# Optimization experiments

Measured on AMD Instinct MI355X. Metric: run time of the kernel, lower is better.

The kernel has to match this reference:

```python
import jax, jax.numpy as jnp
import numpy as np

N, E, IN_C, HID, OUT_C, L = 50000, 800000, 256, 96, 64, 3
DELTAS = (1.0, 0.5, 0.25)


def setup_inputs() -> dict:
    key = jax.random.key(0)
    ks = jax.random.split(key, 10)
    x = jax.random.normal(ks[0], (N, IN_C), dtype=jnp.float32)
    edge_index = jax.random.randint(ks[1], (2, E), 0, N, dtype=jnp.int64)
    s = 1.0 / np.sqrt(IN_C)
    proj_w = jax.random.uniform(ks[2], (IN_C, HID), jnp.float32, -s, s)
    proj_b = jax.random.uniform(ks[3], (HID,), jnp.float32, -s, s)
    sh = 1.0 / np.sqrt(HID)
    conv_w = jax.random.uniform(ks[4], (L, HID, HID), jnp.float32, -sh, sh)
    conv_b = jnp.zeros((L, HID), dtype=jnp.float32)
    so = 1.0 / np.sqrt(2 * HID)
    out_w = jax.random.uniform(ks[5], (2 * HID, OUT_C), jnp.float32, -so, so)
    out_b = jax.random.uniform(ks[6], (OUT_C,), jnp.float32, -so, so)
    # dithered-quantization uniform noise in (-0.5, 0.5), per layer
    b_noise = jax.random.uniform(ks[7], (L, N, HID), jnp.float32) - 0.5
    # additive gaussian noise, per layer
    eps_noise = jax.random.normal(ks[8], (L, N, HID), dtype=jnp.float32) * 0.01
    return {
        "x": x, "edge_index": edge_index,
        "proj_w": proj_w, "proj_b": proj_b,
        "conv_w": conv_w, "conv_b": conv_b,
        "out_w": out_w, "out_b": out_b,
        "b_noise": b_noise, "eps_noise": eps_noise,
    }


def _gcn_norm(edge_index, n):
    # add self-loops and compute symmetric normalization (PyG gcn_norm)
    loops = jnp.arange(n, dtype=edge_index.dtype)
    src = jnp.concatenate([edge_index[0], loops])
    dst = jnp.concatenate([edge_index[1], loops])
    deg = jax.ops.segment_sum(jnp.ones_like(dst, dtype=jnp.float32), dst, num_segments=n)
    dis = jnp.where(deg > 0, jax.lax.rsqrt(jnp.maximum(deg, 1.0)), 0.0)
    norm = dis[src] * dis[dst]  # [E+N]
    return src, dst, norm


def reference(x, edge_index, proj_w, proj_b, conv_w, conv_b, out_w, out_b, b_noise, eps_noise):
    n = x.shape[0]
    src, dst, norm = _gcn_norm(edge_index, n)
    h0 = x @ proj_w + proj_b  # [N, HID]
    h = h0
    for k in range(L):
        delta = DELTAS[k]
        b = b_noise[k] * delta
        h_q = jnp.floor((h + b) / delta) * delta - b  # dithered quantize
        m = h_q @ conv_w[k]                           # [N, HID]
        agg = jax.ops.segment_sum(m[src] * norm[:, None], dst, num_segments=n)
        h = jax.nn.relu(agg + conv_b[k] + eps_noise[k])
    return jnp.concatenate([h0, h], axis=-1) @ out_w + out_b
```

## Files before the change

### kernel.cpp

```cpp
#include <hip/hip_runtime.h>
#include <math.h>

#define N_NODES 50000
#define N_EDGES 800000
#define IN_C    256
#define HID     96
#define OUT_C   64
#define NLAYER  3
#define KC      96
#define XSP     100


__global__ void k_init(int* cnt, int* cur, int* counter,
                       int* col, float* wgt, int n) {
    int v = blockIdx.x * blockDim.x + threadIdx.x;
    if (v < n) { cnt[v] = 0; cur[v] = 0; }
    if (v == 0) *counter = 0;
    if (v < 8) { col[N_EDGES + v] = 0; wgt[N_EDGES + v] = 0.f; }
}

__global__ void k_count(const int* __restrict__ ei, int* cnt, int e) {
    int i = blockIdx.x * blockDim.x + threadIdx.x;
    if (i < e) atomicAdd(&cnt[ei[e + i]], 1);
}

__global__ void k_node(const int* __restrict__ cnt, float* __restrict__ dis,
                       int* __restrict__ start, int* counter, int n) {
    int v = blockIdx.x * blockDim.x + threadIdx.x;
    if (v < n) {
        int c = cnt[v];
        dis[v] = (float)(1.0 / sqrt((double)(c + 1)));
        start[v] = atomicAdd(counter, c);
    }
}

__global__ void k_fill(const int* __restrict__ ei, const float* __restrict__ dis,
                       const int* __restrict__ start, int* __restrict__ cur,
                       int* __restrict__ col, float* __restrict__ wgt, int e) {
    int i = blockIdx.x * blockDim.x + threadIdx.x;
    if (i < e) {
        int s = ei[i];
        int d = ei[e + i];
        int slot = start[d] + atomicAdd(&cur[d], 1);
        col[slot] = s;
        wgt[slot] = dis[s] * dis[d];
    }
}


template<bool QUANT, bool BIAS>
__global__ __launch_bounds__(384) void k_gemm(
    const float* __restrict__ A, int lda, int K,
    const float* __restrict__ bn, float delta, float inv_delta,
    const float* __restrict__ W, const float* __restrict__ bias,
    float* __restrict__ C)
{
    __shared__ float xs[64 * XSP];
    const int t  = threadIdx.x;
    const int og = t % 24;
    const int rg = t / 24;
    const int nch = (K + KC - 1) / KC;
    const int ngroups = (N_NODES + 63) / 64;

    const float* Wt = W + 4 * og;

    float4 bv = make_float4(0.f, 0.f, 0.f, 0.f);
    if (BIAS) bv = *(const float4*)&bias[4 * og];

    for (int g = blockIdx.x; g < ngroups; g += gridDim.x) {
        float acc[4][4];
        #pragma unroll
        for (int r = 0; r < 4; r++)
            #pragma unroll
            for (int o = 0; o < 4; o++) acc[r][o] = 0.f;

        for (int ch = 0; ch < nch; ch++) {
            const int kc0 = ch * KC;
            const int kcw = (K - kc0 < KC) ? (K - kc0) : KC;
            __syncthreads();
            const int kq4 = kcw >> 2;
            const int tot = 64 * kq4;
            for (int i = t; i < tot; i += 384) {
                int node, kq;
                if (kq4 == 24) { node = i / 24; kq = i - node * 24; }
                else           { node = i >> 4; kq = i & 15; }
                int gn = g * 64 + node;
                float4 v = make_float4(0.f, 0.f, 0.f, 0.f);
                if (gn < N_NODES) {
                    v = *(const float4*)&A[(size_t)gn * lda + kc0 + 4 * kq];
                    if (QUANT) {
                        float4 b = *(const float4*)&bn[(size_t)gn * HID + kc0 + 4 * kq];
                        float bx = b.x * delta, by = b.y * delta;
                        float bz = b.z * delta, bw = b.w * delta;
                        v.x = floorf((v.x + bx) * inv_delta) * delta - bx;
                        v.y = floorf((v.y + by) * inv_delta) * delta - by;
                        v.z = floorf((v.z + bz) * inv_delta) * delta - bz;
                        v.w = floorf((v.w + bw) * inv_delta) * delta - bw;
                    }
                }
                *(float4*)&xs[node * XSP + 4 * kq] = v;
            }
            __syncthreads();
            const float* Wc = Wt + (size_t)kc0 * HID;
            for (int k = 0; k < kcw; k += 4) {
                float4 w0 = *(const float4*)&Wc[(size_t)(k + 0) * HID];
                float4 w1 = *(const float4*)&Wc[(size_t)(k + 1) * HID];
                float4 w2 = *(const float4*)&Wc[(size_t)(k + 2) * HID];
                float4 w3 = *(const float4*)&Wc[(size_t)(k + 3) * HID];
                #pragma unroll
                for (int r = 0; r < 4; r++) {
                    float4 xv = *(const float4*)&xs[(4 * rg + r) * XSP + k];
                    acc[r][0] = fmaf(xv.x, w0.x, acc[r][0]);
                    acc[r][1] = fmaf(xv.x, w0.y, acc[r][1]);
                    acc[r][2] = fmaf(xv.x, w0.z, acc[r][2]);
                    acc[r][3] = fmaf(xv.x, w0.w, acc[r][3]);
                    acc[r][0] = fmaf(xv.y, w1.x, acc[r][0]);
                    acc[r][1] = fmaf(xv.y, w1.y, acc[r][1]);
                    acc[r][2] = fmaf(xv.y, w1.z, acc[r][2]);
                    acc[r][3] = fmaf(xv.y, w1.w, acc[r][3]);
                    acc[r][0] = fmaf(xv.z, w2.x, acc[r][0]);
                    acc[r][1] = fmaf(xv.z, w2.y, acc[r][1]);
                    acc[r][2] = fmaf(xv.z, w2.z, acc[r][2]);
                    acc[r][3] = fmaf(xv.z, w2.w, acc[r][3]);
                    acc[r][0] = fmaf(xv.w, w3.x, acc[r][0]);
                    acc[r][1] = fmaf(xv.w, w3.y, acc[r][1]);
                    acc[r][2] = fmaf(xv.w, w3.z, acc[r][2]);
                    acc[r][3] = fmaf(xv.w, w3.w, acc[r][3]);
                }
            }
        }
        #pragma unroll
        for (int r = 0; r < 4; r++) {
            int gn = g * 64 + 4 * rg + r;
            if (gn < N_NODES) {
                float4 c;
                c.x = acc[r][0] + bv.x;
                c.y = acc[r][1] + bv.y;
                c.z = acc[r][2] + bv.z;
                c.w = acc[r][3] + bv.w;
                *(float4*)&C[(size_t)gn * HID + 4 * og] = c;
            }
        }
    }
}


__global__ __launch_bounds__(384) void k_agg(const float* __restrict__ m,
                                             const int* __restrict__ col,
                                             const float* __restrict__ wgt,
                                             const int* __restrict__ start,
                                             const int* __restrict__ cnt,
                                             const float* __restrict__ dis,
                                             const float* __restrict__ cb,
                                             const float* __restrict__ eps,
                                             float* __restrict__ hout) {
    const int tx = threadIdx.x;
    const int d = blockIdx.x * 4 + threadIdx.y;
    const int s0 = start[d], c = cnt[d];
    const float* mt = m + tx;
    float a0 = 0.f, a1 = 0.f, a2 = 0.f, a3 = 0.f;
    float a4 = 0.f, a5 = 0.f, a6 = 0.f, a7 = 0.f;
    for (int e = 0; e < c; e += 8) {
        int i0 = col[s0 + e + 0]; float w0 = (e + 0 < c) ? wgt[s0 + e + 0] : 0.f;
        int i1 = col[s0 + e + 1]; float w1 = (e + 1 < c) ? wgt[s0 + e + 1] : 0.f;
        int i2 = col[s0 + e + 2]; float w2 = (e + 2 < c) ? wgt[s0 + e + 2] : 0.f;
        int i3 = col[s0 + e + 3]; float w3 = (e + 3 < c) ? wgt[s0 + e + 3] : 0.f;
        int i4 = col[s0 + e + 4]; float w4 = (e + 4 < c) ? wgt[s0 + e + 4] : 0.f;
        int i5 = col[s0 + e + 5]; float w5 = (e + 5 < c) ? wgt[s0 + e + 5] : 0.f;
        int i6 = col[s0 + e + 6]; float w6 = (e + 6 < c) ? wgt[s0 + e + 6] : 0.f;
        int i7 = col[s0 + e + 7]; float w7 = (e + 7 < c) ? wgt[s0 + e + 7] : 0.f;
        a0 = fmaf(mt[i0 * HID], w0, a0);
        a1 = fmaf(mt[i1 * HID], w1, a1);
        a2 = fmaf(mt[i2 * HID], w2, a2);
        a3 = fmaf(mt[i3 * HID], w3, a3);
        a4 = fmaf(mt[i4 * HID], w4, a4);
        a5 = fmaf(mt[i5 * HID], w5, a5);
        a6 = fmaf(mt[i6 * HID], w6, a6);
        a7 = fmaf(mt[i7 * HID], w7, a7);
    }
    float dv = dis[d];
    float a = ((a0 + a1) + (a2 + a3)) + ((a4 + a5) + (a6 + a7));
    a = fmaf(mt[d * HID], dv * dv, a);
    a += cb[tx] + eps[(size_t)d * HID + tx];
    hout[(size_t)d * HID + tx] = fmaxf(a, 0.f);
}


__global__ __launch_bounds__(256) void k_out(const float* __restrict__ h0,
                                             const float* __restrict__ h,
                                             const float* __restrict__ W,
                                             const float* __restrict__ bias,
                                             float* __restrict__ out) {
    __shared__ float Ws[2 * HID * OUT_C];
    __shared__ float cs[4][2 * HID];
    int tx = threadIdx.x, ty = threadIdx.y;
    int t = ty * OUT_C + tx;
    for (int i = t; i < 2 * HID * OUT_C; i += 256) Ws[i] = W[i];
    __syncthreads();
    const int ng = N_NODES / 4;
    for (int g = blockIdx.x; g < ng; g += gridDim.x) {
        int r = g * 4 + ty;
        for (int i = tx; i < HID; i += OUT_C) {
            cs[ty][i] = h0[r * HID + i];
            cs[ty][HID + i] = h[r * HID + i];
        }
        __syncthreads();
        float a = 0.f;
        #pragma unroll 16
        for (int i = 0; i < 2 * HID; i++) a = fmaf(cs[ty][i], Ws[i * OUT_C + tx], a);
        out[r * OUT_C + tx] = a + bias[tx];
        __syncthreads();
    }
}


extern "C" void kernel_launch(void* const* d_in, const int* in_sizes, int n_in,
                              void* d_out, int out_size, void* d_ws, size_t ws_size,
                              hipStream_t stream) {
    (void)in_sizes; (void)n_in; (void)out_size; (void)ws_size;
    const float* x       = (const float*)d_in[0];
    const int*   ei      = (const int*)d_in[1];
    const float* proj_w  = (const float*)d_in[2];
    const float* proj_b  = (const float*)d_in[3];
    const float* conv_w  = (const float*)d_in[4];
    const float* conv_b  = (const float*)d_in[5];
    const float* out_w   = (const float*)d_in[6];
    const float* out_b   = (const float*)d_in[7];
    const float* b_noise = (const float*)d_in[8];
    const float* eps_n   = (const float*)d_in[9];
    float*       out     = (float*)d_out;

    char* w = (char*)d_ws;
    size_t off = 0;
    auto alloc = [&](size_t bytes) -> char* {
        char* p = w + off;
        off = (off + bytes + 255) & ~(size_t)255;
        return p;
    };
    float* h0b   = (float*)alloc((size_t)N_NODES * HID * 4);
    float* hA    = (float*)alloc((size_t)N_NODES * HID * 4);
    float* mb    = (float*)alloc((size_t)N_NODES * HID * 4);
    float* dis   = (float*)alloc((size_t)N_NODES * 4);
    float* wgt   = (float*)alloc((size_t)(N_EDGES + 8) * 4);
    int*   col   = (int*)  alloc((size_t)(N_EDGES + 8) * 4);
    int*   cnt   = (int*)  alloc((size_t)N_NODES * 4);
    int*   cur   = (int*)  alloc((size_t)N_NODES * 4);
    int*   start = (int*)  alloc((size_t)N_NODES * 4);
    int*   ctr   = (int*)  alloc(256);

    k_init <<<(N_NODES + 255) / 256, 256, 0, stream>>>(cnt, cur, ctr, col, wgt, N_NODES);
    k_count<<<(N_EDGES + 255) / 256, 256, 0, stream>>>(ei, cnt, N_EDGES);
    k_node <<<(N_NODES + 255) / 256, 256, 0, stream>>>(cnt, dis, start, ctr, N_NODES);
    k_fill <<<(N_EDGES + 255) / 256, 256, 0, stream>>>(ei, dis, start, cur, col, wgt, N_EDGES);

    const int ngroups = (N_NODES + 63) / 64;

    k_gemm<false, true><<<ngroups, 384, 0, stream>>>(
        x, IN_C, IN_C, nullptr, 1.f, 1.f, proj_w, proj_b, h0b);

    const float deltas[NLAYER] = {1.0f, 0.5f, 0.25f};
    const float* hprev = h0b;
    for (int k = 0; k < NLAYER; k++) {
        float dlt = deltas[k];
        k_gemm<true, false><<<ngroups, 384, 0, stream>>>(
            hprev, HID, HID,
            b_noise + (size_t)k * N_NODES * HID, dlt, 1.0f / dlt,
            conv_w + (size_t)k * HID * HID, nullptr, mb);
        k_agg<<<N_NODES / 4, dim3(96, 4), 0, stream>>>(
            mb, col, wgt, start, cnt, dis,
            conv_b + (size_t)k * HID,
            eps_n + (size_t)k * N_NODES * HID, hA);
        hprev = hA;
    }

    k_out<<<1024, dim3(64, 4), 0, stream>>>(h0b, hprev, out_w, out_b, out);
}
```

Measured before the change: 672.7 us.

## Batch GEMM tile loads, double-buffer weights, widen aggregation unroll, register-tile output GEMM

New measurement: 670.1 us. No clear change (-0.4%).

```diff
diff --git a/kernel.cpp b/kernel.cpp
--- a/kernel.cpp
+++ b/kernel.cpp
@@ -10,13 +10,19 @@
 #define KC      96
 #define XSP     100
 
+#define FMA_ROW(xv, w0, w1, w2, w3, AR) \
+    AR[0]=fmaf(xv.x,w0.x,AR[0]); AR[1]=fmaf(xv.x,w0.y,AR[1]); AR[2]=fmaf(xv.x,w0.z,AR[2]); AR[3]=fmaf(xv.x,w0.w,AR[3]); \
+    AR[0]=fmaf(xv.y,w1.x,AR[0]); AR[1]=fmaf(xv.y,w1.y,AR[1]); AR[2]=fmaf(xv.y,w1.z,AR[2]); AR[3]=fmaf(xv.y,w1.w,AR[3]); \
+    AR[0]=fmaf(xv.z,w2.x,AR[0]); AR[1]=fmaf(xv.z,w2.y,AR[1]); AR[2]=fmaf(xv.z,w2.z,AR[2]); AR[3]=fmaf(xv.z,w2.w,AR[3]); \
+    AR[0]=fmaf(xv.w,w3.x,AR[0]); AR[1]=fmaf(xv.w,w3.y,AR[1]); AR[2]=fmaf(xv.w,w3.z,AR[2]); AR[3]=fmaf(xv.w,w3.w,AR[3]);
+
 
 __global__ void k_init(int* cnt, int* cur, int* counter,
                        int* col, float* wgt, int n) {
     int v = blockIdx.x * blockDim.x + threadIdx.x;
     if (v < n) { cnt[v] = 0; cur[v] = 0; }
     if (v == 0) *counter = 0;
-    if (v < 8) { col[N_EDGES + v] = 0; wgt[N_EDGES + v] = 0.f; }
+    if (v < 16) { col[N_EDGES + v] = 0; wgt[N_EDGES + v] = 0.f; }
 }
 
 __global__ void k_count(const int* __restrict__ ei, int* cnt, int e) {
@@ -77,55 +83,82 @@
         for (int ch = 0; ch < nch; ch++) {
             const int kc0 = ch * KC;
             const int kcw = (K - kc0 < KC) ? (K - kc0) : KC;
+            const int kq4 = kcw >> 2;
             __syncthreads();
-            const int kq4 = kcw >> 2;
-            const int tot = 64 * kq4;
-            for (int i = t; i < tot; i += 384) {
-                int node, kq;
-                if (kq4 == 24) { node = i / 24; kq = i - node * 24; }
-                else           { node = i >> 4; kq = i & 15; }
-                int gn = g * 64 + node;
-                float4 v = make_float4(0.f, 0.f, 0.f, 0.f);
-                if (gn < N_NODES) {
-                    v = *(const float4*)&A[(size_t)gn * lda + kc0 + 4 * kq];
+            if (kq4 == 24) {
+                float4 va[4], vb[4];
+                int nd[4], kq[4];
+                #pragma unroll
+                for (int j = 0; j < 4; j++) {
+                    int i = t + 384 * j;
+                    nd[j] = i / 24; kq[j] = i - nd[j] * 24;
+                    int gn = g * 64 + nd[j];
+                    int gc = gn < N_NODES ? gn : N_NODES - 1;
+                    va[j] = *(const float4*)&A[(size_t)gc * lda + kc0 + 4 * kq[j]];
+                    if (QUANT)
+                        vb[j] = *(const float4*)&bn[(size_t)gc * HID + kc0 + 4 * kq[j]];
+                }
+                #pragma unroll
+                for (int j = 0; j < 4; j++) {
+                    float4 v = va[j];
                     if (QUANT) {
-                        float4 b = *(const float4*)&bn[(size_t)gn * HID + kc0 + 4 * kq];
-                        float bx = b.x * delta, by = b.y * delta;
-                        float bz = b.z * delta, bw = b.w * delta;
+                        float bx = vb[j].x * delta, by = vb[j].y * delta;
+                        float bz = vb[j].z * delta, bw = vb[j].w * delta;
                         v.x = floorf((v.x + bx) * inv_delta) * delta - bx;
                         v.y = floorf((v.y + by) * inv_delta) * delta - by;
                         v.z = floorf((v.z + bz) * inv_delta) * delta - bz;
                         v.w = floorf((v.w + bw) * inv_delta) * delta - bw;
                     }
-                }
-                *(float4*)&xs[node * XSP + 4 * kq] = v;
+                    if (g * 64 + nd[j] >= N_NODES) v = make_float4(0.f, 0.f, 0.f, 0.f);
+                    *(float4*)&xs[nd[j] * XSP + 4 * kq[j]] = v;
+                }
+            } else {
+                const int tot = 64 * kq4;
+                for (int i = t; i < tot; i += 384) {
+                    int node = i >> 4, kq = i & 15;
+                    int gn = g * 64 + node;
+                    float4 v = make_float4(0.f, 0.f, 0.f, 0.f);
+                    if (gn < N_NODES) {
+                        v = *(const float4*)&A[(size_t)gn * lda + kc0 + 4 * kq];
+                        if (QUANT) {
+                            float4 b = *(const float4*)&bn[(size_t)gn * HID + kc0 + 4 * kq];
+                            float bx = b.x * delta, by = b.y * delta;
+                            float bz = b.z * delta, bw = b.w * delta;
+                            v.x = floorf((v.x + bx) * inv_delta) * delta - bx;
+                            v.y = floorf((v.y + by) * inv_delta) * delta - by;
+                            v.z = floorf((v.z + bz) * inv_delta) * delta - bz;
+                            v.w = floorf((v.w + bw) * inv_delta) * delta - bw;
+                        }
+                    }
+                    *(float4*)&xs[node * XSP + 4 * kq] = v;
+                }
             }
             __syncthreads();
             const float* Wc = Wt + (size_t)kc0 * HID;
-            for (int k = 0; k < kcw; k += 4) {
-                float4 w0 = *(const float4*)&Wc[(size_t)(k + 0) * HID];
-                float4 w1 = *(const float4*)&Wc[(size_t)(k + 1) * HID];
-                float4 w2 = *(const float4*)&Wc[(size_t)(k + 2) * HID];
-                float4 w3 = *(const float4*)&Wc[(size_t)(k + 3) * HID];
+            float4 wa0 = *(const float4*)&Wc[0 * HID];
+            float4 wa1 = *(const float4*)&Wc[1 * HID];
+            float4 wa2 = *(const float4*)&Wc[2 * HID];
+            float4 wa3 = *(const float4*)&Wc[3 * HID];
+            for (int k = 0; k < kcw; k += 8) {
+                float4 wb0 = *(const float4*)&Wc[(k + 4) * HID];
+                float4 wb1 = *(const float4*)&Wc[(k + 5) * HID];
+                float4 wb2 = *(const float4*)&Wc[(k + 6) * HID];
+                float4 wb3 = *(const float4*)&Wc[(k + 7) * HID];
                 #pragma unroll
                 for (int r = 0; r < 4; r++) {
                     float4 xv = *(const float4*)&xs[(4 * rg + r) * XSP + k];
-                    acc[r][0] = fmaf(xv.x, w0.x, acc[r][0]);
-                    acc[r][1] = fmaf(xv.x, w0.y, acc[r][1]);
-                    acc[r][2] = fmaf(xv.x, w0.z, acc[r][2]);
-                    acc[r][3] = fmaf(xv.x, w0.w, acc[r][3]);
-                    acc[r][0] = fmaf(xv.y, w1.x, acc[r][0]);
-                    acc[r][1] = fmaf(xv.y, w1.y, acc[r][1]);
-                    acc[r][2] = fmaf(xv.y, w1.z, acc[r][2]);
-                    acc[r][3] = fmaf(xv.y, w1.w, acc[r][3]);
-                    acc[r][0] = fmaf(xv.z, w2.x, acc[r][0]);
-                    acc[r][1] = fmaf(xv.z, w2.y, acc[r][1]);
-                    acc[r][2] = fmaf(xv.z, w2.z, acc[r][2]);
-                    acc[r][3] = fmaf(xv.z, w2.w, acc[r][3]);
-                    acc[r][0] = fmaf(xv.w, w3.x, acc[r][0]);
-                    acc[r][1] = fmaf(xv.w, w3.y, acc[r][1]);
-                    acc[r][2] = fmaf(xv.w, w3.z, acc[r][2]);
-                    acc[r][3] = fmaf(xv.w, w3.w, acc[r][3]);
+                    FMA_ROW(xv, wa0, wa1, wa2, wa3, acc[r]);
+                }
+                if (k + 8 < kcw) {
+                    wa0 = *(const float4*)&Wc[(k + 8)  * HID];
+                    wa1 = *(const float4*)&Wc[(k + 9)  * HID];
+                    wa2 = *(const float4*)&Wc[(k + 10) * HID];
+                    wa3 = *(const float4*)&Wc[(k + 11) * HID];
+                }
+                #pragma unroll
+                for (int r = 0; r < 4; r++) {
+                    float4 xv = *(const float4*)&xs[(4 * rg + r) * XSP + k + 4];
+                    FMA_ROW(xv, wb0, wb1, wb2, wb3, acc[r]);
                 }
             }
         }
@@ -158,58 +191,109 @@
     const int d = blockIdx.x * 4 + threadIdx.y;
     const int s0 = start[d], c = cnt[d];
     const float* mt = m + tx;
-    float a0 = 0.f, a1 = 0.f, a2 = 0.f, a3 = 0.f;
-    float a4 = 0.f, a5 = 0.f, a6 = 0.f, a7 = 0.f;
-    for (int e = 0; e < c; e += 8) {
-        int i0 = col[s0 + e + 0]; float w0 = (e + 0 < c) ? wgt[s0 + e + 0] : 0.f;
-        int i1 = col[s0 + e + 1]; float w1 = (e + 1 < c) ? wgt[s0 + e + 1] : 0.f;
-        int i2 = col[s0 + e + 2]; float w2 = (e + 2 < c) ? wgt[s0 + e + 2] : 0.f;
-        int i3 = col[s0 + e + 3]; float w3 = (e + 3 < c) ? wgt[s0 + e + 3] : 0.f;
-        int i4 = col[s0 + e + 4]; float w4 = (e + 4 < c) ? wgt[s0 + e + 4] : 0.f;
-        int i5 = col[s0 + e + 5]; float w5 = (e + 5 < c) ? wgt[s0 + e + 5] : 0.f;
-        int i6 = col[s0 + e + 6]; float w6 = (e + 6 < c) ? wgt[s0 + e + 6] : 0.f;
-        int i7 = col[s0 + e + 7]; float w7 = (e + 7 < c) ? wgt[s0 + e + 7] : 0.f;
-        a0 = fmaf(mt[i0 * HID], w0, a0);
-        a1 = fmaf(mt[i1 * HID], w1, a1);
-        a2 = fmaf(mt[i2 * HID], w2, a2);
-        a3 = fmaf(mt[i3 * HID], w3, a3);
-        a4 = fmaf(mt[i4 * HID], w4, a4);
-        a5 = fmaf(mt[i5 * HID], w5, a5);
-        a6 = fmaf(mt[i6 * HID], w6, a6);
-        a7 = fmaf(mt[i7 * HID], w7, a7);
+    float a[8];
+    #pragma unroll
+    for (int j = 0; j < 8; j++) a[j] = 0.f;
+    for (int e = 0; e < c; e += 16) {
+        int   idx[16];
+        float wv[16];
+        #pragma unroll
+        for (int j = 0; j < 16; j++) {
+            idx[j] = col[s0 + e + j];
+            wv[j]  = (e + j < c) ? wgt[s0 + e + j] : 0.f;
+        }
+        #pragma unroll
+        for (int j = 0; j < 16; j++)
+            a[j & 7] = fmaf(mt[idx[j] * HID], wv[j], a[j & 7]);
     }
     float dv = dis[d];
-    float a = ((a0 + a1) + (a2 + a3)) + ((a4 + a5) + (a6 + a7));
-    a = fmaf(mt[d * HID], dv * dv, a);
-    a += cb[tx] + eps[(size_t)d * HID + tx];
-    hout[(size_t)d * HID + tx] = fmaxf(a, 0.f);
-}
-
-
-__global__ __launch_bounds__(256) void k_out(const float* __restrict__ h0,
-                                             const float* __restrict__ h,
-                                             const float* __restrict__ W,
-                                             const float* __restrict__ bias,
-                                             float* __restrict__ out) {
-    __shared__ float Ws[2 * HID * OUT_C];
-    __shared__ float cs[4][2 * HID];
-    int tx = threadIdx.x, ty = threadIdx.y;
-    int t = ty * OUT_C + tx;
-    for (int i = t; i < 2 * HID * OUT_C; i += 256) Ws[i] = W[i];
-    __syncthreads();
-    const int ng = N_NODES / 4;
-    for (int g = blockIdx.x; g < ng; g += gridDim.x) {
-        int r = g * 4 + ty;
-        for (int i = tx; i < HID; i += OUT_C) {
-            cs[ty][i] = h0[r * HID + i];
-            cs[ty][HID + i] = h[r * HID + i];
-        }
-        __syncthreads();
-        float a = 0.f;
-        #pragma unroll 16
-        for (int i = 0; i < 2 * HID; i++) a = fmaf(cs[ty][i], Ws[i * OUT_C + tx], a);
-        out[r * OUT_C + tx] = a + bias[tx];
-        __syncthreads();
+    float s = ((a[0] + a[1]) + (a[2] + a[3])) + ((a[4] + a[5]) + (a[6] + a[7]));
+    s = fmaf(mt[d * HID], dv * dv, s);
+    s += cb[tx] + eps[(size_t)d * HID + tx];
+    hout[(size_t)d * HID + tx] = fmaxf(s, 0.f);
+}
+
+
+__global__ __launch_bounds__(384) void k_out2(const float* __restrict__ h0,
+                                              const float* __restrict__ h,
+                                              const float* __restrict__ W,
+                                              const float* __restrict__ bias,
+                                              float* __restrict__ out) {
+    __shared__ float xs[96 * XSP];
+    const int t  = threadIdx.x;
+    const int og = t % 16;
+    const int rg = t / 16;
+    const int ngroups = (N_NODES + 95) / 96;
+
+    const float* Wt = W + 4 * og;
+    float4 bv = *(const float4*)&bias[4 * og];
+
+    for (int g = blockIdx.x; g < ngroups; g += gridDim.x) {
+        float acc[4][4];
+        #pragma unroll
+        for (int r = 0; r < 4; r++)
+            #pragma unroll
+            for (int o = 0; o < 4; o++) acc[r][o] = 0.f;
+
+        #pragma unroll
+        for (int ch = 0; ch < 2; ch++) {
+            const float* src = ch ? h : h0;
+            __syncthreads();
+            float4 va[6];
+            int nd[6], kq[6];
+            #pragma unroll
+            for (int j = 0; j < 6; j++) {
+                int i = t + 384 * j;
+                nd[j] = i / 24; kq[j] = i - nd[j] * 24;
+                int gn = g * 96 + nd[j];
+                int gc = gn < N_NODES ? gn : N_NODES - 1;
+                va[j] = *(const float4*)&src[(size_t)gc * HID + 4 * kq[j]];
+            }
+            #pragma unroll
+            for (int j = 0; j < 6; j++)
+                *(float4*)&xs[nd[j] * XSP + 4 * kq[j]] = va[j];
+            __syncthreads();
+
+            const float* Wc = Wt + (size_t)(ch * HID) * OUT_C;
+            float4 wa0 = *(const float4*)&Wc[0 * OUT_C];
+            float4 wa1 = *(const float4*)&Wc[1 * OUT_C];
+            float4 wa2 = *(const float4*)&Wc[2 * OUT_C];
+            float4 wa3 = *(const float4*)&Wc[3 * OUT_C];
+            for (int k = 0; k < HID; k += 8) {
+                float4 wb0 = *(const float4*)&Wc[(k + 4) * OUT_C];
+                float4 wb1 = *(const float4*)&Wc[(k + 5) * OUT_C];
+                float4 wb2 = *(const float4*)&Wc[(k + 6) * OUT_C];
+                float4 wb3 = *(const float4*)&Wc[(k + 7) * OUT_C];
+                #pragma unroll
+                for (int r = 0; r < 4; r++) {
+                    float4 xv = *(const float4*)&xs[(4 * rg + r) * XSP + k];
+                    FMA_ROW(xv, wa0, wa1, wa2, wa3, acc[r]);
+                }
+                if (k + 8 < HID) {
+                    wa0 = *(const float4*)&Wc[(k + 8)  * OUT_C];
+                    wa1 = *(const float4*)&Wc[(k + 9)  * OUT_C];
+                    wa2 = *(const float4*)&Wc[(k + 10) * OUT_C];
+                    wa3 = *(const float4*)&Wc[(k + 11) * OUT_C];
+                }
+                #pragma unroll
+                for (int r = 0; r < 4; r++) {
+                    float4 xv = *(const float4*)&xs[(4 * rg + r) * XSP + k + 4];
+                    FMA_ROW(xv, wb0, wb1, wb2, wb3, acc[r]);
+                }
+            }
+        }
+        #pragma unroll
+        for (int r = 0; r < 4; r++) {
+            int gn = g * 96 + 4 * rg + r;
+            if (gn < N_NODES) {
+                float4 c;
+                c.x = acc[r][0] + bv.x;
+                c.y = acc[r][1] + bv.y;
+                c.z = acc[r][2] + bv.z;
+                c.w = acc[r][3] + bv.w;
+                *(float4*)&out[(size_t)gn * OUT_C + 4 * og] = c;
+            }
+        }
     }
 }
 
@@ -241,8 +325,8 @@
     float* hA    = (float*)alloc((size_t)N_NODES * HID * 4);
     float* mb    = (float*)alloc((size_t)N_NODES * HID * 4);
     float* dis   = (float*)alloc((size_t)N_NODES * 4);
-    float* wgt   = (float*)alloc((size_t)(N_EDGES + 8) * 4);
-    int*   col   = (int*)  alloc((size_t)(N_EDGES + 8) * 4);
+    float* wgt   = (float*)alloc((size_t)(N_EDGES + 16) * 4);
+    int*   col   = (int*)  alloc((size_t)(N_EDGES + 16) * 4);
     int*   cnt   = (int*)  alloc((size_t)N_NODES * 4);
     int*   cur   = (int*)  alloc((size_t)N_NODES * 4);
     int*   start = (int*)  alloc((size_t)N_NODES * 4);
@@ -273,5 +357,6 @@
         hprev = hA;
     }
 
-    k_out<<<1024, dim3(64, 4), 0, stream>>>(h0b, hprev, out_w, out_b, out);
-}
+    const int ogroups = (N_NODES + 95) / 96;
+    k_out2<<<ogroups, 384, 0, stream>>>(h0b, hprev, out_w, out_b, out);
+}
```
